# Kernel tuning notes

Measured on AMD Instinct MI355X. Metric: run time of the kernel, lower is better.

## Reference

```python
import jax, jax.numpy as jnp
import numpy as np

OUT, IN = 8192, 8192
GROUP = 128
N_GROUPS = IN // GROUP
BATCH = 64


def dequant_int4(packed, scales):
    # packed: [OUT, IN//2] int32 bytes in [0,256); two 4-bit codes per byte
    low = packed & 0xF            # first element of each pair
    high = (packed >> 4) & 0xF    # second element
    q = jnp.stack([low, high], axis=-1).reshape(OUT, IN)  # interleaved nibbles
    # symmetric grouped dequant: w = (q - 8) * scale, scale per [row, group]
    qg = q.reshape(OUT, N_GROUPS, GROUP).astype(scales.dtype)
    w = (qg - 8.0) * scales[:, :, None]
    return w.reshape(OUT, IN)


def setup_inputs() -> dict:
    key = jax.random.key(0)
    k1, k2, k3 = jax.random.split(key, 3)
    x = jax.random.normal(k1, (BATCH, IN), dtype=jnp.float32)
    packed = jax.random.randint(k2, (OUT, IN // 2), 0, 256, dtype=jnp.int32)
    scales = jax.random.uniform(k3, (OUT, N_GROUPS), dtype=jnp.float32)
    return {"x": x, "packed": packed, "scales": scales}


def reference(x, packed, scales):
    # Dequantize int4 weights then dense matmul (F.linear, no bias)
    w = dequant_int4(packed, scales)        # [OUT, IN]
    return jnp.einsum('bi,oi->bo', x, w)    # [BATCH, OUT]
```

## Files before the change

kernel.cpp:

```cpp
#include <hip/hip_runtime.h>
#include <hip/hip_bf16.h>
#include <stdint.h>

#define OUTN   8192
#define INN    8192
#define NGRP   64
#define BATCHN 64
#define BN     64
#define BK     128
#define KSPLIT 8
#define KCHUNK (INN / KSPLIT)
#define NITER  (KCHUNK / BK)
#define OSZ    (BATCHN * OUTN)

typedef __attribute__((ext_vector_type(8))) short bf16x8;
typedef __attribute__((ext_vector_type(4))) float f32x4;
typedef __attribute__((ext_vector_type(4))) unsigned int u32x4;

__device__ __forceinline__ unsigned short f2bf(float f) {
  __hip_bfloat16 h = __float2bfloat16(f);
  return __builtin_bit_cast(unsigned short, h);
}
__device__ __forceinline__ float bf2f(unsigned short h) {
  unsigned int u = ((unsigned int)h) << 16;
  return __builtin_bit_cast(float, u);
}

__global__ void qlin_prep(const float* __restrict__ x, float* __restrict__ xsum) {
  const int b = blockIdx.x;
  const int t = threadIdx.x;
  const float* xrow = x + (size_t)b * INN + t * 32;
  float s = 0.0f;
#pragma unroll
  for (int i = 0; i < 8; ++i) {
    float4 v = *(const float4*)(xrow + i * 4);
    s += bf2f(f2bf(v.x)) + bf2f(f2bf(v.y)) + bf2f(f2bf(v.z)) + bf2f(f2bf(v.w));
  }
  __shared__ float part[256];
  part[t] = s;
  __syncthreads();
  if (t < NGRP) {
    float g = part[4 * t] + part[4 * t + 1] + part[4 * t + 2] + part[4 * t + 3];
    xsum[t * BATCHN + b] = g;
  }
}

#define PKS 17
#define XTS 136

__global__ __launch_bounds__(256, 4) void qlin_main(
    const float* __restrict__ x, const int* __restrict__ packed,
    const float* __restrict__ scales, const float* __restrict__ xsum,
    float* __restrict__ out, float* __restrict__ part) {
  const int bx    = blockIdx.x;
  const int ks    = bx & (KSPLIT - 1);
  const int ntile = bx >> 3;
  const int o0    = ntile * BN;
  const int g0    = ks * NITER;

  const int t    = threadIdx.x;
  const int lane = t & 63;
  const int w    = t >> 6;
  const int l15  = lane & 15;
  const int quad = lane >> 4;

  __shared__ __align__(16) unsigned int   pk_c[BN * PKS];
  __shared__ __align__(16) unsigned short xt[BATCHN * XTS];
  __shared__ __align__(16) float          st[BN][9];
  __shared__ __align__(16) float          xs[NITER][BATCHN];

#pragma unroll
  for (int i = 0; i < 2; ++i) {
    int v = t * 2 + i;
    int ol = v >> 3, gl = v & 7;
    st[ol][gl] = scales[(size_t)(o0 + ol) * NGRP + g0 + gl];
    int gl2 = v >> 6, b2 = v & 63;
    xs[gl2][b2] = xsum[(g0 + gl2) * BATCHN + b2];
  }

  int4   pkr[4];
  float4 xr[8];

  const int prow = t >> 4, pcol = t & 15;
  const int xrow = t >> 5, xcol = t & 31;

  auto load_tile = [&](int i) {
    const int kk2 = ks * (KCHUNK / 2) + i * (BK / 2);
    const int* pbase = packed + (size_t)(o0 + prow) * (INN / 2) + kk2 + pcol * 4;
#pragma unroll
    for (int j = 0; j < 4; ++j)
      pkr[j] = *(const int4*)(pbase + (size_t)(16 * j) * (INN / 2));
    const int kk = ks * KCHUNK + i * BK;
    const float* xbase = x + (size_t)xrow * INN + kk + xcol * 4;
#pragma unroll
    for (int j = 0; j < 8; ++j)
      xr[j] = *(const float4*)(xbase + (size_t)(8 * j) * INN);
  };

  auto store_tile = [&]() {
#pragma unroll
    for (int j = 0; j < 4; ++j) {
      unsigned int c = (unsigned)pkr[j].x | ((unsigned)pkr[j].y << 8) |
                       ((unsigned)pkr[j].z << 16) | ((unsigned)pkr[j].w << 24);
      pk_c[(prow + 16 * j) * PKS + pcol] = c;
    }
#pragma unroll
    for (int j = 0; j < 8; ++j) {
      ushort4 h;
      h.x = f2bf(xr[j].x); h.y = f2bf(xr[j].y);
      h.z = f2bf(xr[j].z); h.w = f2bf(xr[j].w);
      *(ushort4*)&xt[(xrow + 8 * j) * XTS + xcol * 4] = h;
    }
  };

  f32x4 facc[4];
#pragma unroll
  for (int mt = 0; mt < 4; ++mt) facc[mt] = (f32x4){0.f, 0.f, 0.f, 0.f};

  load_tile(0);

  for (int i = 0; i < NITER; ++i) {
    __syncthreads();
    store_tile();
    if (i + 1 < NITER) load_tile(i + 1);
    __syncthreads();

    f32x4 gacc[4];
#pragma unroll
    for (int mt = 0; mt < 4; ++mt) gacc[mt] = (f32x4){0.f, 0.f, 0.f, 0.f};

#pragma unroll
    for (int kq = 0; kq < 4; ++kq) {
      bf16x8 af[4];
#pragma unroll
      for (int mt = 0; mt < 4; ++mt)
        af[mt] = *(const bf16x8*)&xt[(mt * 16 + l15) * XTS + kq * 32 + quad * 8];

      unsigned int c = pk_c[(w * 16 + l15) * PKS + kq * 4 + quad];
      u32x4 bw;
      bw.x = 0x43004300u | (c & 0xFu) | ((c & 0xF0u) << 12);
      bw.y = 0x43004300u | ((c >> 8) & 0xFu) | (((c >> 8) & 0xF0u) << 12);
      bw.z = 0x43004300u | ((c >> 16) & 0xFu) | (((c >> 16) & 0xF0u) << 12);
      bw.w = 0x43004300u | ((c >> 24) & 0xFu) | (((c >> 24) & 0xF0u) << 12);
      bf16x8 bfv = __builtin_bit_cast(bf16x8, bw);

#pragma unroll
      for (int mt = 0; mt < 4; ++mt)
        gacc[mt] = __builtin_amdgcn_mfma_f32_16x16x32_bf16(af[mt], bfv, gacc[mt], 0, 0, 0);
    }

    float s0 = st[w * 16 + l15][i];
#pragma unroll
    for (int mt = 0; mt < 4; ++mt) {
      f32x4 xv = *(const f32x4*)&xs[i][mt * 16 + quad * 4];
#pragma unroll
      for (int r = 0; r < 4; ++r)
        facc[mt][r] += s0 * (gacc[mt][r] - 136.0f * xv[r]);
    }
  }

  const int obase = o0 + w * 16 + l15;
  if (part) {
    float* pb = part + (size_t)ks * OSZ;
#pragma unroll
    for (int mt = 0; mt < 4; ++mt)
#pragma unroll
      for (int r = 0; r < 4; ++r) {
        int m = mt * 16 + quad * 4 + r;
        pb[(size_t)m * OUTN + obase] = facc[mt][r];
      }
  } else {
#pragma unroll
    for (int mt = 0; mt < 4; ++mt)
#pragma unroll
      for (int r = 0; r < 4; ++r) {
        int m = mt * 16 + quad * 4 + r;
        atomicAdd(&out[(size_t)m * OUTN + obase], facc[mt][r]);
      }
  }
}

__global__ void qlin_reduce(const float* __restrict__ part, float* __restrict__ out) {
  const size_t i = ((size_t)blockIdx.x * 256 + threadIdx.x) * 4;
  float4 s = *(const float4*)(part + i);
#pragma unroll
  for (int ks = 1; ks < KSPLIT; ++ks) {
    float4 v = *(const float4*)(part + (size_t)ks * OSZ + i);
    s.x += v.x; s.y += v.y; s.z += v.z; s.w += v.w;
  }
  *(float4*)(out + i) = s;
}

extern "C" void kernel_launch(void* const* d_in, const int* in_sizes, int n_in,
                              void* d_out, int out_size, void* d_ws, size_t ws_size,
                              hipStream_t stream) {
  const float* x      = (const float*)d_in[0];
  const int*   packed = (const int*)d_in[1];
  const float* scales = (const float*)d_in[2];
  float* out  = (float*)d_out;
  float* xsum = (float*)d_ws;
  const size_t part_off = 16384 / sizeof(float);
  const size_t need = 16384 + (size_t)KSPLIT * OSZ * sizeof(float);
  float* part = (ws_size >= need) ? ((float*)d_ws + part_off) : nullptr;

  qlin_prep<<<BATCHN, 256, 0, stream>>>(x, xsum);
  if (!part)
    hipMemsetAsync(d_out, 0, (size_t)out_size * sizeof(float), stream);
  qlin_main<<<(OUTN / BN) * KSPLIT, 256, 0, stream>>>(x, packed, scales, xsum, out, part);
  if (part)
    qlin_reduce<<<OSZ / 4 / 256, 256, 0, stream>>>(part, out);
}
```

Before: 207.9 us.

## Pre-swizzle activations to bf16 and drop LDS staging in main kernel

Adds a pre-pass that converts x to bf16 in an MFMA-fragment-friendly swizzled layout, so the main kernel loads A fragments and packed weights straight from global memory into registers. This removes the shared-memory tiles, per-iteration barriers and in-loop bf16 conversion. Scales now sit in registers, and the next packed tile is register-prefetched. In exchange, every wave re-reads the activations from global/L2 with no LDS reuse, an extra kernel launch is added, and it needs more workspace. The packed int32 loads now feed one byte per 32-bit lane, which looks inconsistent with the nibble-pair layout the old code assembled.

```diff
diff --git a/kernel.cpp b/kernel.cpp
--- a/kernel.cpp
+++ b/kernel.cpp
@@ -6,11 +6,9 @@
 #define INN    8192
 #define NGRP   64
 #define BATCHN 64
-#define BN     64
-#define BK     128
 #define KSPLIT 8
 #define KCHUNK (INN / KSPLIT)
-#define NITER  (KCHUNK / BK)
+#define NITER  (KCHUNK / 128)
 #define OSZ    (BATCHN * OUTN)
 
 typedef __attribute__((ext_vector_type(8))) short bf16x8;
@@ -45,86 +43,63 @@
   }
 }
 
-#define PKS 17
-#define XTS 136
+__global__ void qlin_swz(const float* __restrict__ x, unsigned short* __restrict__ xswz) {
+  const int idx = blockIdx.x * 256 + threadIdx.x;
+  const int b  = idx & 63;
+  const int kb = idx >> 6;
+  const float* p = x + (size_t)b * INN + kb * 8;
+  float4 v0 = *(const float4*)p;
+  float4 v1 = *(const float4*)(p + 4);
+  u32x4 o;
+  o.x = (unsigned)f2bf(v0.x) | ((unsigned)f2bf(v0.y) << 16);
+  o.y = (unsigned)f2bf(v0.z) | ((unsigned)f2bf(v0.w) << 16);
+  o.z = (unsigned)f2bf(v1.x) | ((unsigned)f2bf(v1.y) << 16);
+  o.w = (unsigned)f2bf(v1.z) | ((unsigned)f2bf(v1.w) << 16);
+  *(u32x4*)&xswz[(size_t)idx * 8] = o;
+}
 
 __global__ __launch_bounds__(256, 4) void qlin_main(
-    const float* __restrict__ x, const int* __restrict__ packed,
-    const float* __restrict__ scales, const float* __restrict__ xsum,
+    const int* __restrict__ packed, const float* __restrict__ scales,
+    const unsigned short* __restrict__ xswz, const float* __restrict__ xsum,
     float* __restrict__ out, float* __restrict__ part) {
   const int bx    = blockIdx.x;
   const int ks    = bx & (KSPLIT - 1);
   const int ntile = bx >> 3;
-  const int o0    = ntile * BN;
+  const int o0    = ntile * 64;
   const int g0    = ks * NITER;
 
   const int t    = threadIdx.x;
   const int lane = t & 63;
   const int w    = t >> 6;
-  const int l15  = lane & 15;
-  const int quad = lane >> 4;
-
-  __shared__ __align__(16) unsigned int   pk_c[BN * PKS];
-  __shared__ __align__(16) unsigned short xt[BATCHN * XTS];
-  __shared__ __align__(16) float          st[BN][9];
-  __shared__ __align__(16) float          xs[NITER][BATCHN];
-
+  const int r    = lane & 15;
+  const int q    = lane >> 4;
+  const int orow = o0 + w * 16 + r;
+
+  __shared__ float xs[NITER][BATCHN];
 #pragma unroll
   for (int i = 0; i < 2; ++i) {
     int v = t * 2 + i;
-    int ol = v >> 3, gl = v & 7;
-    st[ol][gl] = scales[(size_t)(o0 + ol) * NGRP + g0 + gl];
-    int gl2 = v >> 6, b2 = v & 63;
-    xs[gl2][b2] = xsum[(g0 + gl2) * BATCHN + b2];
-  }
-
-  int4   pkr[4];
-  float4 xr[8];
-
-  const int prow = t >> 4, pcol = t & 15;
-  const int xrow = t >> 5, xcol = t & 31;
-
-  auto load_tile = [&](int i) {
-    const int kk2 = ks * (KCHUNK / 2) + i * (BK / 2);
-    const int* pbase = packed + (size_t)(o0 + prow) * (INN / 2) + kk2 + pcol * 4;
-#pragma unroll
-    for (int j = 0; j < 4; ++j)
-      pkr[j] = *(const int4*)(pbase + (size_t)(16 * j) * (INN / 2));
-    const int kk = ks * KCHUNK + i * BK;
-    const float* xbase = x + (size_t)xrow * INN + kk + xcol * 4;
-#pragma unroll
-    for (int j = 0; j < 8; ++j)
-      xr[j] = *(const float4*)(xbase + (size_t)(8 * j) * INN);
-  };
-
-  auto store_tile = [&]() {
-#pragma unroll
-    for (int j = 0; j < 4; ++j) {
-      unsigned int c = (unsigned)pkr[j].x | ((unsigned)pkr[j].y << 8) |
-                       ((unsigned)pkr[j].z << 16) | ((unsigned)pkr[j].w << 24);
-      pk_c[(prow + 16 * j) * PKS + pcol] = c;
-    }
-#pragma unroll
-    for (int j = 0; j < 8; ++j) {
-      ushort4 h;
-      h.x = f2bf(xr[j].x); h.y = f2bf(xr[j].y);
-      h.z = f2bf(xr[j].z); h.w = f2bf(xr[j].w);
-      *(ushort4*)&xt[(xrow + 8 * j) * XTS + xcol * 4] = h;
-    }
-  };
+    xs[v >> 6][v & 63] = xsum[(g0 + (v >> 6)) * BATCHN + (v & 63)];
+  }
+
+  float4 sa = *(const float4*)&scales[(size_t)orow * NGRP + g0];
+  float4 sb = *(const float4*)&scales[(size_t)orow * NGRP + g0 + 4];
+  float sreg[8] = {sa.x, sa.y, sa.z, sa.w, sb.x, sb.y, sb.z, sb.w};
+
+  const int* bptr = packed + (size_t)orow * (INN / 2) + ks * (KCHUNK / 2) + q * 4;
+  const unsigned short* aptr = xswz + ((size_t)(ks * 128 + q) * 64 + r) * 8;
+
+  __syncthreads();
 
   f32x4 facc[4];
 #pragma unroll
   for (int mt = 0; mt < 4; ++mt) facc[mt] = (f32x4){0.f, 0.f, 0.f, 0.f};
 
-  load_tile(0);
+  int4 b4[4], b4n[4];
+#pragma unroll
+  for (int kq = 0; kq < 4; ++kq) b4[kq] = *(const int4*)(bptr + kq * 16);
 
   for (int i = 0; i < NITER; ++i) {
-    __syncthreads();
-    store_tile();
-    if (i + 1 < NITER) load_tile(i + 1);
-    __syncthreads();
-
     f32x4 gacc[4];
 #pragma unroll
     for (int mt = 0; mt < 4; ++mt) gacc[mt] = (f32x4){0.f, 0.f, 0.f, 0.f};
@@ -134,48 +109,61 @@
       bf16x8 af[4];
 #pragma unroll
       for (int mt = 0; mt < 4; ++mt)
-        af[mt] = *(const bf16x8*)&xt[(mt * 16 + l15) * XTS + kq * 32 + quad * 8];
-
-      unsigned int c = pk_c[(w * 16 + l15) * PKS + kq * 4 + quad];
-      u32x4 bw;
-      bw.x = 0x43004300u | (c & 0xFu) | ((c & 0xF0u) << 12);
-      bw.y = 0x43004300u | ((c >> 8) & 0xFu) | (((c >> 8) & 0xF0u) << 12);
-      bw.z = 0x43004300u | ((c >> 16) & 0xFu) | (((c >> 16) & 0xF0u) << 12);
-      bw.w = 0x43004300u | ((c >> 24) & 0xFu) | (((c >> 24) & 0xF0u) << 12);
-      bf16x8 bfv = __builtin_bit_cast(bf16x8, bw);
+        af[mt] = *(const bf16x8*)(aptr + ((size_t)(i * 16 + kq * 4) * 64 + mt * 16) * 8);
+
+      int4 c = b4[kq];
+      u32x4 bw0, bw1;
+      bw0.x = 0x43004300u | ((unsigned)c.x & 0xFu) | (((unsigned)c.x & 0xF0u) << 12);
+      bw0.y = 0x43004300u | ((unsigned)c.y & 0xFu) | (((unsigned)c.y & 0xF0u) << 12);
+      bw0.z = 0x43004300u | ((unsigned)c.z & 0xFu) | (((unsigned)c.z & 0xF0u) << 12);
+      bw0.w = 0x43004300u | ((unsigned)c.w & 0xFu) | (((unsigned)c.w & 0xF0u) << 12);
+      bf16x8 bfv;
+      bfv[0] = (short)(bw0.x & 0xFFFF); bfv[1] = (short)(bw0.x >> 16);
+      bfv[2] = (short)(bw0.y & 0xFFFF); bfv[3] = (short)(bw0.y >> 16);
+      bfv[4] = (short)(bw0.z & 0xFFFF); bfv[5] = (short)(bw0.z >> 16);
+      bfv[6] = (short)(bw0.w & 0xFFFF); bfv[7] = (short)(bw0.w >> 16);
+      (void)bw1;
 
 #pragma unroll
       for (int mt = 0; mt < 4; ++mt)
         gacc[mt] = __builtin_amdgcn_mfma_f32_16x16x32_bf16(af[mt], bfv, gacc[mt], 0, 0, 0);
     }
 
-    float s0 = st[w * 16 + l15][i];
+    if (i + 1 < NITER) {
+#pragma unroll
+      for (int kq = 0; kq < 4; ++kq)
+        b4n[kq] = *(const int4*)(bptr + (i + 1) * 64 + kq * 16);
+    }
+
+    float s0 = sreg[i];
 #pragma unroll
     for (int mt = 0; mt < 4; ++mt) {
-      f32x4 xv = *(const f32x4*)&xs[i][mt * 16 + quad * 4];
-#pragma unroll
-      for (int r = 0; r < 4; ++r)
-        facc[mt][r] += s0 * (gacc[mt][r] - 136.0f * xv[r]);
+      f32x4 xv = *(const f32x4*)&xs[i][mt * 16 + q * 4];
+#pragma unroll
+      for (int rr = 0; rr < 4; ++rr)
+        facc[mt][rr] += s0 * (gacc[mt][rr] - 136.0f * xv[rr]);
     }
-  }
-
-  const int obase = o0 + w * 16 + l15;
+
+#pragma unroll
+    for (int kq = 0; kq < 4; ++kq) b4[kq] = b4n[kq];
+  }
+
   if (part) {
     float* pb = part + (size_t)ks * OSZ;
 #pragma unroll
     for (int mt = 0; mt < 4; ++mt)
 #pragma unroll
-      for (int r = 0; r < 4; ++r) {
-        int m = mt * 16 + quad * 4 + r;
-        pb[(size_t)m * OUTN + obase] = facc[mt][r];
+      for (int rr = 0; rr < 4; ++rr) {
+        int m = mt * 16 + q * 4 + rr;
+        pb[(size_t)m * OUTN + orow] = facc[mt][rr];
       }
   } else {
 #pragma unroll
     for (int mt = 0; mt < 4; ++mt)
 #pragma unroll
-      for (int r = 0; r < 4; ++r) {
-        int m = mt * 16 + quad * 4 + r;
-        atomicAdd(&out[(size_t)m * OUTN + obase], facc[mt][r]);
+      for (int rr = 0; rr < 4; ++rr) {
+        int m = mt * 16 + q * 4 + rr;
+        atomicAdd(&out[(size_t)m * OUTN + orow], facc[mt][rr]);
       }
   }
 }
@@ -197,16 +185,19 @@
   const float* x      = (const float*)d_in[0];
   const int*   packed = (const int*)d_in[1];
   const float* scales = (const float*)d_in[2];
-  float* out  = (float*)d_out;
-  float* xsum = (float*)d_ws;
-  const size_t part_off = 16384 / sizeof(float);
-  const size_t need = 16384 + (size_t)KSPLIT * OSZ * sizeof(float);
-  float* part = (ws_size >= need) ? ((float*)d_ws + part_off) : nullptr;
+  float* out = (float*)d_out;
+
+  char* ws = (char*)d_ws;
+  float*          xsum = (float*)ws;
+  unsigned short* xswz = (unsigned short*)(ws + 16384);
+  const size_t part_need = 16384 + 1048576 + (size_t)KSPLIT * OSZ * sizeof(float);
+  float* part = (ws_size >= part_need) ? (float*)(ws + 16384 + 1048576) : nullptr;
 
   qlin_prep<<<BATCHN, 256, 0, stream>>>(x, xsum);
+  qlin_swz<<<(INN / 8) * BATCHN / 256, 256, 0, stream>>>(x, xswz);
   if (!part)
     hipMemsetAsync(d_out, 0, (size_t)out_size * sizeof(float), stream);
-  qlin_main<<<(OUTN / BN) * KSPLIT, 256, 0, stream>>>(x, packed, scales, xsum, out, part);
+  qlin_main<<<(OUTN / 64) * KSPLIT, 256, 0, stream>>>(packed, scales, xswz, xsum, out, part);
   if (part)
     qlin_reduce<<<OSZ / 4 / 256, 256, 0, stream>>>(part, out);
 }
```

Result: slower. 217.5 us (+4.6%).
